# Kernel optimization log

Measured on AMD Instinct MI355X. Metric: run time of the kernel, lower is better.

The kernel has to match this reference:

```python
import jax, jax.numpy as jnp
import numpy as np

DILATION = 64
KERNEL = 2

def setup_inputs() -> dict:
    key = jax.random.key(0)
    k1, k2 = jax.random.split(key)
    x = jax.random.normal(k1, (16, 64, 16384), dtype=jnp.float32)
    w = jax.random.normal(k2, (64, 64, KERNEL), dtype=jnp.float32) * 0.1
    return {"x": x, "w": w}

def _causal_dilated_conv(x, w):
    # left-pad by dilation*(kernel_size-1) for causality
    pad = DILATION * (KERNEL - 1)
    xp = jnp.pad(x, ((0, 0), (0, 0), (pad, 0)))
    return jax.lax.conv_general_dilated(
        xp, w,
        window_strides=(1,),
        padding='VALID',
        rhs_dilation=(DILATION,),
        dimension_numbers=('NCH', 'OIH', 'NCH'))

def reference(x, w):
    y = _causal_dilated_conv(x, w)          # [B, C_out, T]
    return jnp.tanh(y) * jax.nn.sigmoid(y)  # fused gate
```

## Files before the change

### kernel.cpp

```cpp
#include <hip/hip_runtime.h>


#define B_ 16
#define C_ 64
#define T_ 16384
#define TT 128
#define HALO 64
#define RR (TT + HALO)

typedef __attribute__((ext_vector_type(8))) short short8;
typedef __attribute__((ext_vector_type(4))) float f32x4;

union Frag { short8 s; unsigned u[4]; };

__device__ __forceinline__ unsigned bf16_rne(float f) {
    unsigned u = __float_as_uint(f);
    return (u + 0x7fffu + ((u >> 16) & 1u)) >> 16;
}

__device__ __forceinline__ unsigned pack_rne(float a, float b) {
    unsigned ua = __float_as_uint(a), ub = __float_as_uint(b);
    unsigned ra = ua + 0x7fffu + ((ua >> 16) & 1u);
    unsigned rb = ub + 0x7fffu + ((ub >> 16) & 1u);
    return (ra >> 16) | (rb & 0xffff0000u);
}

__global__ __launch_bounds__(256, 6) void conv_gate_mfma3(
    const float* __restrict__ x,
    const float* __restrict__ w,
    float* __restrict__ out)
{
    __shared__ unsigned short xs[RR * 64];

    const int tid = threadIdx.x;
    const int t0  = blockIdx.x * TT;
    const int b   = blockIdx.y;
    const float* xb = x + (size_t)b * C_ * T_;

    #pragma unroll
    for (int it = 0; it < 6; ++it) {
        int task = it * 256 + tid;
        int rr   = task % RR;
        int c8   = task / RR;
        int g    = t0 - HALO + rr;
        float v[8];
        if (g >= 0) {
            const float* xp = xb + (size_t)(8 * c8) * T_ + g;
            #pragma unroll
            for (int i = 0; i < 8; ++i) v[i] = xp[(size_t)i * T_];
        } else {
            #pragma unroll
            for (int i = 0; i < 8; ++i) v[i] = 0.f;
        }
        unsigned p0 = pack_rne(v[0], v[1]);
        unsigned p1 = pack_rne(v[2], v[3]);
        unsigned p2 = pack_rne(v[4], v[5]);
        unsigned p3 = pack_rne(v[6], v[7]);
        int so = rr * 64 + ((c8 ^ (rr & 7)) * 8);
        *(uint4*)(&xs[so]) = make_uint4(p0, p1, p2, p3);
    }

    const int lane = tid & 63;
    const int wid  = tid >> 6;
    const int m    = lane & 15;
    const int q    = lane >> 4;
    const int co   = wid * 16 + m;

    Frag wh[2][2], wl[2][2];
    #pragma unroll
    for (int h = 0; h < 2; ++h) {
        const float* wp = w + co * 128 + h * 64 + q * 16;
        float f[16];
        #pragma unroll
        for (int v4 = 0; v4 < 4; ++v4) {
            float4 t4 = *(const float4*)(wp + 4 * v4);
            f[4*v4+0] = t4.x; f[4*v4+1] = t4.y; f[4*v4+2] = t4.z; f[4*v4+3] = t4.w;
        }
        #pragma unroll
        for (int p = 0; p < 2; ++p) {
            #pragma unroll
            for (int d = 0; d < 4; ++d) {
                float e0 = f[2*(2*d)   + p];
                float e1 = f[2*(2*d+1) + p];
                unsigned h0 = bf16_rne(e0), h1 = bf16_rne(e1);
                float r0 = e0 - __uint_as_float(h0 << 16);
                float r1 = e1 - __uint_as_float(h1 << 16);
                wh[p][h].u[d] = h0 | (h1 << 16);
                wl[p][h].u[d] = bf16_rne(r0) | (bf16_rne(r1) << 16);
            }
        }
    }

    f32x4 acc[8];
    #pragma unroll
    for (int s = 0; s < 8; ++s) acc[s] = (f32x4){0.f, 0.f, 0.f, 0.f};

    __syncthreads();

    const int n  = m;
    const int sw = n & 7;
    #pragma unroll
    for (int u = 0; u < 12; ++u) {
        const int rbase = (16 * u + n) * 64;
        Frag f0, f1;
        f0.s = *(const short8*)(&xs[rbase + ((q ^ sw) * 8)]);
        f1.s = *(const short8*)(&xs[rbase + (((4 + q) ^ sw) * 8)]);
        if (u < 8) {
            acc[u] = __builtin_amdgcn_mfma_f32_16x16x32_bf16(wh[0][0].s, f0.s, acc[u], 0, 0, 0);
            acc[u] = __builtin_amdgcn_mfma_f32_16x16x32_bf16(wl[0][0].s, f0.s, acc[u], 0, 0, 0);
            acc[u] = __builtin_amdgcn_mfma_f32_16x16x32_bf16(wh[0][1].s, f1.s, acc[u], 0, 0, 0);
            acc[u] = __builtin_amdgcn_mfma_f32_16x16x32_bf16(wl[0][1].s, f1.s, acc[u], 0, 0, 0);
        }
        if (u >= 4) {
            const int s2 = u - 4;
            acc[s2] = __builtin_amdgcn_mfma_f32_16x16x32_bf16(wh[1][0].s, f0.s, acc[s2], 0, 0, 0);
            acc[s2] = __builtin_amdgcn_mfma_f32_16x16x32_bf16(wl[1][0].s, f0.s, acc[s2], 0, 0, 0);
            acc[s2] = __builtin_amdgcn_mfma_f32_16x16x32_bf16(wh[1][1].s, f1.s, acc[s2], 0, 0, 0);
            acc[s2] = __builtin_amdgcn_mfma_f32_16x16x32_bf16(wl[1][1].s, f1.s, acc[s2], 0, 0, 0);
        }
    }

    float* ob = out + ((size_t)b * C_ + wid * 16) * T_ + t0;
    #pragma unroll
    for (int s = 0; s < 8; ++s) {
        #pragma unroll
        for (int r = 0; r < 4; ++r) {
            float y  = acc[s][r];
            y = fminf(fmaxf(y, -20.f), 20.f);
            float e   = __expf(-y);
            float e2  = e * e;
            float num = 1.f - e2;
            float den = (1.f + e) * (1.f + e2);
            ob[(size_t)(4 * q + r) * T_ + 16 * s + n] = num * __builtin_amdgcn_rcpf(den);
        }
    }
}

extern "C" void kernel_launch(void* const* d_in, const int* in_sizes, int n_in,
                              void* d_out, int out_size, void* d_ws, size_t ws_size,
                              hipStream_t stream) {
    const float* x = (const float*)d_in[0];
    const float* w = (const float*)d_in[1];
    float* out = (float*)d_out;
    dim3 grid(T_ / TT, B_);
    conv_gate_mfma3<<<grid, dim3(256), 0, stream>>>(x, w, out);
}
```

Before: 123.8 us.

## Stream time tiles through an LDS ring buffer with software-pipelined loads

Each block now handles 256 time steps in four 64-step chunks. It keeps a 128-row LDS ring, so the 64-sample halo is reused instead of reloaded. Global loads for the next chunk are issued before the MFMAs of the current chunk, and the previous chunk's gate epilogue is interleaved with them. Block IDs are remapped to spread work across XCDs. This cuts the halo re-read overhead and overlaps memory with compute, at the cost of extra barriers, higher register pressure (occupancy hint lowered to 4) and fewer blocks (1024).

```diff
diff --git a/kernel.cpp b/kernel.cpp
--- a/kernel.cpp
+++ b/kernel.cpp
@@ -4,9 +4,7 @@
 #define B_ 16
 #define C_ 64
 #define T_ 16384
-#define TT 128
-#define HALO 64
-#define RR (TT + HALO)
+#define RING 128
 
 typedef __attribute__((ext_vector_type(8))) short short8;
 typedef __attribute__((ext_vector_type(4))) float f32x4;
@@ -25,39 +23,52 @@
     return (ra >> 16) | (rb & 0xffff0000u);
 }
 
-__global__ __launch_bounds__(256, 6) void conv_gate_mfma3(
+#define EPILOGUE(A, KK)                                                     \
+    _Pragma("unroll")                                                       \
+    for (int s = 0; s < 4; ++s) {                                           \
+        _Pragma("unroll")                                                   \
+        for (int r = 0; r < 4; ++r) {                                       \
+            float y = (A)[s][r];                                            \
+            y = fminf(fmaxf(y, -20.f), 20.f);                               \
+            float e   = __expf(-y);                                         \
+            float e2  = e * e;                                              \
+            float num = 1.f - e2;                                           \
+            float den = (1.f + e) * (1.f + e2);                             \
+            ob[(size_t)(4 * q + r) * T_ + ((KK) * 64 + 16 * s + n)] =       \
+                num * __builtin_amdgcn_rcpf(den);                           \
+        }                                                                   \
+    }
+
+__global__ __launch_bounds__(256, 4) void conv_gate_ring(
     const float* __restrict__ x,
     const float* __restrict__ w,
     float* __restrict__ out)
 {
-    __shared__ unsigned short xs[RR * 64];
+    __shared__ unsigned short xs[RING * 64];
 
     const int tid = threadIdx.x;
-    const int t0  = blockIdx.x * TT;
-    const int b   = blockIdx.y;
+    const int bid = blockIdx.x;
+    const int wg  = (bid & 7) * 128 + (bid >> 3);
+    const int b   = wg >> 6;
+    const int seg = wg & 63;
+    const int t0  = seg << 8;
     const float* xb = x + (size_t)b * C_ * T_;
 
+    float pv[4][8];
     #pragma unroll
-    for (int it = 0; it < 6; ++it) {
-        int task = it * 256 + tid;
-        int rr   = task % RR;
-        int c8   = task / RR;
-        int g    = t0 - HALO + rr;
-        float v[8];
+    for (int it = 0; it < 4; ++it) {
+        const int task = it * 256 + tid;
+        const int rr   = task & 127;
+        const int c8   = task >> 7;
+        const int g    = t0 - 64 + rr;
         if (g >= 0) {
             const float* xp = xb + (size_t)(8 * c8) * T_ + g;
             #pragma unroll
-            for (int i = 0; i < 8; ++i) v[i] = xp[(size_t)i * T_];
+            for (int i = 0; i < 8; ++i) pv[it][i] = xp[(size_t)i * T_];
         } else {
             #pragma unroll
-            for (int i = 0; i < 8; ++i) v[i] = 0.f;
+            for (int i = 0; i < 8; ++i) pv[it][i] = 0.f;
         }
-        unsigned p0 = pack_rne(v[0], v[1]);
-        unsigned p1 = pack_rne(v[2], v[3]);
-        unsigned p2 = pack_rne(v[4], v[5]);
-        unsigned p3 = pack_rne(v[6], v[7]);
-        int so = rr * 64 + ((c8 ^ (rr & 7)) * 8);
-        *(uint4*)(&xs[so]) = make_uint4(p0, p1, p2, p3);
     }
 
     const int lane = tid & 63;
@@ -91,49 +102,89 @@
         }
     }
 
-    f32x4 acc[8];
     #pragma unroll
-    for (int s = 0; s < 8; ++s) acc[s] = (f32x4){0.f, 0.f, 0.f, 0.f};
+    for (int it = 0; it < 4; ++it) {
+        const int task = it * 256 + tid;
+        const int rr   = task & 127;
+        const int c8   = task >> 7;
+        unsigned p0 = pack_rne(pv[it][0], pv[it][1]);
+        unsigned p1 = pack_rne(pv[it][2], pv[it][3]);
+        unsigned p2 = pack_rne(pv[it][4], pv[it][5]);
+        unsigned p3 = pack_rne(pv[it][6], pv[it][7]);
+        const int slot = (rr + 64) & 127;
+        const int so   = slot * 64 + ((c8 ^ (rr & 7)) * 8);
+        *(uint4*)(&xs[so]) = make_uint4(p0, p1, p2, p3);
+    }
+
+    const int n   = m;
+    const int swb = n & 7;
+    float* ob = out + ((size_t)b * C_ + wid * 16) * T_ + t0;
+
+    f32x4 acc2[2][4];
 
     __syncthreads();
 
-    const int n  = m;
-    const int sw = n & 7;
     #pragma unroll
-    for (int u = 0; u < 12; ++u) {
-        const int rbase = (16 * u + n) * 64;
-        Frag f0, f1;
-        f0.s = *(const short8*)(&xs[rbase + ((q ^ sw) * 8)]);
-        f1.s = *(const short8*)(&xs[rbase + (((4 + q) ^ sw) * 8)]);
-        if (u < 8) {
-            acc[u] = __builtin_amdgcn_mfma_f32_16x16x32_bf16(wh[0][0].s, f0.s, acc[u], 0, 0, 0);
-            acc[u] = __builtin_amdgcn_mfma_f32_16x16x32_bf16(wl[0][0].s, f0.s, acc[u], 0, 0, 0);
-            acc[u] = __builtin_amdgcn_mfma_f32_16x16x32_bf16(wh[0][1].s, f1.s, acc[u], 0, 0, 0);
-            acc[u] = __builtin_amdgcn_mfma_f32_16x16x32_bf16(wl[0][1].s, f1.s, acc[u], 0, 0, 0);
+    for (int k = 0; k < 4; ++k) {
+        float v[2][8];
+        if (k < 3) {
+            #pragma unroll
+            for (int it = 0; it < 2; ++it) {
+                const int task = it * 256 + tid;
+                const int rr = task & 63, c8 = task >> 6;
+                const float* xp = xb + (size_t)(8 * c8) * T_ + (t0 + 64 * (k + 1) + rr);
+                #pragma unroll
+                for (int i = 0; i < 8; ++i) v[it][i] = xp[(size_t)i * T_];
+            }
         }
-        if (u >= 4) {
-            const int s2 = u - 4;
-            acc[s2] = __builtin_amdgcn_mfma_f32_16x16x32_bf16(wh[1][0].s, f0.s, acc[s2], 0, 0, 0);
-            acc[s2] = __builtin_amdgcn_mfma_f32_16x16x32_bf16(wl[1][0].s, f0.s, acc[s2], 0, 0, 0);
-            acc[s2] = __builtin_amdgcn_mfma_f32_16x16x32_bf16(wh[1][1].s, f1.s, acc[s2], 0, 0, 0);
-            acc[s2] = __builtin_amdgcn_mfma_f32_16x16x32_bf16(wl[1][1].s, f1.s, acc[s2], 0, 0, 0);
+
+        if (k > 0) { EPILOGUE(acc2[(k & 1) ^ 1], k - 1); }
+
+        f32x4* acc = acc2[k & 1];
+        #pragma unroll
+        for (int s = 0; s < 4; ++s) acc[s] = (f32x4){0.f, 0.f, 0.f, 0.f};
+        const int kb = ((k & 1) ^ 1) << 6;
+        #pragma unroll
+        for (int u = 0; u < 8; ++u) {
+            const int rbase = ((kb + 16 * u + n) & 127) * 64;
+            Frag f0, f1;
+            f0.s = *(const short8*)(&xs[rbase + ((q ^ swb) * 8)]);
+            f1.s = *(const short8*)(&xs[rbase + (((4 + q) ^ swb) * 8)]);
+            if (u < 4) {
+                acc[u] = __builtin_amdgcn_mfma_f32_16x16x32_bf16(wh[0][0].s, f0.s, acc[u], 0, 0, 0);
+                acc[u] = __builtin_amdgcn_mfma_f32_16x16x32_bf16(wl[0][0].s, f0.s, acc[u], 0, 0, 0);
+                acc[u] = __builtin_amdgcn_mfma_f32_16x16x32_bf16(wh[0][1].s, f1.s, acc[u], 0, 0, 0);
+                acc[u] = __builtin_amdgcn_mfma_f32_16x16x32_bf16(wl[0][1].s, f1.s, acc[u], 0, 0, 0);
+            } else {
+                const int s2 = u - 4;
+                acc[s2] = __builtin_amdgcn_mfma_f32_16x16x32_bf16(wh[1][0].s, f0.s, acc[s2], 0, 0, 0);
+                acc[s2] = __builtin_amdgcn_mfma_f32_16x16x32_bf16(wl[1][0].s, f0.s, acc[s2], 0, 0, 0);
+                acc[s2] = __builtin_amdgcn_mfma_f32_16x16x32_bf16(wh[1][1].s, f1.s, acc[s2], 0, 0, 0);
+                acc[s2] = __builtin_amdgcn_mfma_f32_16x16x32_bf16(wl[1][1].s, f1.s, acc[s2], 0, 0, 0);
+            }
+        }
+
+        if (k < 3) {
+            __syncthreads();
+
+            #pragma unroll
+            for (int it = 0; it < 2; ++it) {
+                const int task = it * 256 + tid;
+                const int rr = task & 63, c8 = task >> 6;
+                unsigned p0 = pack_rne(v[it][0], v[it][1]);
+                unsigned p1 = pack_rne(v[it][2], v[it][3]);
+                unsigned p2 = pack_rne(v[it][4], v[it][5]);
+                unsigned p3 = pack_rne(v[it][6], v[it][7]);
+                const int slot = (64 * (k + 1) + rr) & 127;
+                const int so   = slot * 64 + ((c8 ^ (rr & 7)) * 8);
+                *(uint4*)(&xs[so]) = make_uint4(p0, p1, p2, p3);
+            }
+
+            __syncthreads();
         }
     }
 
-    float* ob = out + ((size_t)b * C_ + wid * 16) * T_ + t0;
-    #pragma unroll
-    for (int s = 0; s < 8; ++s) {
-        #pragma unroll
-        for (int r = 0; r < 4; ++r) {
-            float y  = acc[s][r];
-            y = fminf(fmaxf(y, -20.f), 20.f);
-            float e   = __expf(-y);
-            float e2  = e * e;
-            float num = 1.f - e2;
-            float den = (1.f + e) * (1.f + e2);
-            ob[(size_t)(4 * q + r) * T_ + 16 * s + n] = num * __builtin_amdgcn_rcpf(den);
-        }
-    }
+    EPILOGUE(acc2[1], 3);
 }
 
 extern "C" void kernel_launch(void* const* d_in, const int* in_sizes, int n_in,
@@ -142,6 +193,5 @@
     const float* x = (const float*)d_in[0];
     const float* w = (const float*)d_in[1];
     float* out = (float*)d_out;
-    dim3 grid(T_ / TT, B_);
-    conv_gate_mfma3<<<grid, dim3(256), 0, stream>>>(x, w, out);
+    conv_gate_ring<<<dim3(1024), dim3(256), 0, stream>>>(x, w, out);
 }
```

After: 126.3 us. About the same (+2.0%).

## Stream x directly into registers with rolling halo, dropping shared-memory staging

Applied to the files above, without the earlier changes.

The conv kernel no longer stages a bf16 tile in LDS. Each wave loads its MFMA B-fragments straight from global memory and keeps the dilated halo in a four-slot rolling register buffer, with a two-deep register prefetch of upcoming columns. Tiles grow to 256 timesteps (1024 blocks on a 1-D grid remapped in XCD-interleaved order), which removes the halo re-read and the __syncthreads barrier. In exchange, register pressure rises (launch bounds drop to 4), and each wave issues strided scalar global loads, so every wave now performs its own global reads.

```diff
diff --git a/kernel.cpp b/kernel.cpp
--- a/kernel.cpp
+++ b/kernel.cpp
@@ -4,9 +4,6 @@
 #define B_ 16
 #define C_ 64
 #define T_ 16384
-#define TT 128
-#define HALO 64
-#define RR (TT + HALO)
 
 typedef __attribute__((ext_vector_type(8))) short short8;
 typedef __attribute__((ext_vector_type(4))) float f32x4;
@@ -25,46 +22,27 @@
     return (ra >> 16) | (rb & 0xffff0000u);
 }
 
-__global__ __launch_bounds__(256, 6) void conv_gate_mfma3(
+__global__ __launch_bounds__(256, 4) void conv_gate_stream(
     const float* __restrict__ x,
     const float* __restrict__ w,
     float* __restrict__ out)
 {
-    __shared__ unsigned short xs[RR * 64];
-
     const int tid = threadIdx.x;
-    const int t0  = blockIdx.x * TT;
-    const int b   = blockIdx.y;
-    const float* xb = x + (size_t)b * C_ * T_;
-
-    #pragma unroll
-    for (int it = 0; it < 6; ++it) {
-        int task = it * 256 + tid;
-        int rr   = task % RR;
-        int c8   = task / RR;
-        int g    = t0 - HALO + rr;
-        float v[8];
-        if (g >= 0) {
-            const float* xp = xb + (size_t)(8 * c8) * T_ + g;
-            #pragma unroll
-            for (int i = 0; i < 8; ++i) v[i] = xp[(size_t)i * T_];
-        } else {
-            #pragma unroll
-            for (int i = 0; i < 8; ++i) v[i] = 0.f;
-        }
-        unsigned p0 = pack_rne(v[0], v[1]);
-        unsigned p1 = pack_rne(v[2], v[3]);
-        unsigned p2 = pack_rne(v[4], v[5]);
-        unsigned p3 = pack_rne(v[6], v[7]);
-        int so = rr * 64 + ((c8 ^ (rr & 7)) * 8);
-        *(uint4*)(&xs[so]) = make_uint4(p0, p1, p2, p3);
-    }
+    const int bid = blockIdx.x;
+    const int wg  = (bid & 7) * 128 + (bid >> 3);
+    const int b   = wg >> 6;
+    const int s   = wg & 63;
+    const int t0  = s << 8;
 
     const int lane = tid & 63;
     const int wid  = tid >> 6;
     const int m    = lane & 15;
     const int q    = lane >> 4;
     const int co   = wid * 16 + m;
+
+    const float* xb  = x + (size_t)b * C_ * T_;
+    const float* xh0 = xb + (size_t)(8 * q) * T_ + m;
+    const float* xh1 = xb + (size_t)(32 + 8 * q) * T_ + m;
 
     Frag wh[2][2], wl[2][2];
     #pragma unroll
@@ -91,47 +69,83 @@
         }
     }
 
-    f32x4 acc[8];
+    Frag pk[4][2];
+    if (s > 0) {
+        #pragma unroll
+        for (int jj = 0; jj < 4; ++jj) {
+            float v0[8], v1[8];
+            const float* p0 = xh0 + (t0 - 64 + 16 * jj);
+            const float* p1 = xh1 + (t0 - 64 + 16 * jj);
+            #pragma unroll
+            for (int i = 0; i < 8; ++i) {
+                v0[i] = p0[(size_t)i * T_];
+                v1[i] = p1[(size_t)i * T_];
+            }
+            #pragma unroll
+            for (int d = 0; d < 4; ++d) {
+                pk[jj][0].u[d] = pack_rne(v0[2*d], v0[2*d+1]);
+                pk[jj][1].u[d] = pack_rne(v1[2*d], v1[2*d+1]);
+            }
+        }
+    } else {
+        #pragma unroll
+        for (int jj = 0; jj < 4; ++jj) {
+            #pragma unroll
+            for (int d = 0; d < 4; ++d) { pk[jj][0].u[d] = 0u; pk[jj][1].u[d] = 0u; }
+        }
+    }
+
+    float fl[2][16];
     #pragma unroll
-    for (int s = 0; s < 8; ++s) acc[s] = (f32x4){0.f, 0.f, 0.f, 0.f};
-
-    __syncthreads();
-
-    const int n  = m;
-    const int sw = n & 7;
-    #pragma unroll
-    for (int u = 0; u < 12; ++u) {
-        const int rbase = (16 * u + n) * 64;
-        Frag f0, f1;
-        f0.s = *(const short8*)(&xs[rbase + ((q ^ sw) * 8)]);
-        f1.s = *(const short8*)(&xs[rbase + (((4 + q) ^ sw) * 8)]);
-        if (u < 8) {
-            acc[u] = __builtin_amdgcn_mfma_f32_16x16x32_bf16(wh[0][0].s, f0.s, acc[u], 0, 0, 0);
-            acc[u] = __builtin_amdgcn_mfma_f32_16x16x32_bf16(wl[0][0].s, f0.s, acc[u], 0, 0, 0);
-            acc[u] = __builtin_amdgcn_mfma_f32_16x16x32_bf16(wh[0][1].s, f1.s, acc[u], 0, 0, 0);
-            acc[u] = __builtin_amdgcn_mfma_f32_16x16x32_bf16(wl[0][1].s, f1.s, acc[u], 0, 0, 0);
-        }
-        if (u >= 4) {
-            const int s2 = u - 4;
-            acc[s2] = __builtin_amdgcn_mfma_f32_16x16x32_bf16(wh[1][0].s, f0.s, acc[s2], 0, 0, 0);
-            acc[s2] = __builtin_amdgcn_mfma_f32_16x16x32_bf16(wl[1][0].s, f0.s, acc[s2], 0, 0, 0);
-            acc[s2] = __builtin_amdgcn_mfma_f32_16x16x32_bf16(wh[1][1].s, f1.s, acc[s2], 0, 0, 0);
-            acc[s2] = __builtin_amdgcn_mfma_f32_16x16x32_bf16(wl[1][1].s, f1.s, acc[s2], 0, 0, 0);
+    for (int jj = 0; jj < 2; ++jj) {
+        const float* p0 = xh0 + (t0 + 16 * jj);
+        const float* p1 = xh1 + (t0 + 16 * jj);
+        #pragma unroll
+        for (int i = 0; i < 8; ++i) {
+            fl[jj][i]     = p0[(size_t)i * T_];
+            fl[jj][8 + i] = p1[(size_t)i * T_];
         }
     }
 
     float* ob = out + ((size_t)b * C_ + wid * 16) * T_ + t0;
+
     #pragma unroll
-    for (int s = 0; s < 8; ++s) {
+    for (int j = 0; j < 16; ++j) {
+        Frag n0, n1;
+        #pragma unroll
+        for (int d = 0; d < 4; ++d) {
+            n0.u[d] = pack_rne(fl[j & 1][2*d],     fl[j & 1][2*d + 1]);
+            n1.u[d] = pack_rne(fl[j & 1][8 + 2*d], fl[j & 1][8 + 2*d + 1]);
+        }
+        if (j < 14) {
+            const float* p0 = xh0 + (t0 + 16 * (j + 2));
+            const float* p1 = xh1 + (t0 + 16 * (j + 2));
+            #pragma unroll
+            for (int i = 0; i < 8; ++i) {
+                fl[j & 1][i]     = p0[(size_t)i * T_];
+                fl[j & 1][8 + i] = p1[(size_t)i * T_];
+            }
+        }
+        f32x4 acc = (f32x4){0.f, 0.f, 0.f, 0.f};
+        acc = __builtin_amdgcn_mfma_f32_16x16x32_bf16(wh[0][0].s, pk[j & 3][0].s, acc, 0, 0, 0);
+        acc = __builtin_amdgcn_mfma_f32_16x16x32_bf16(wl[0][0].s, pk[j & 3][0].s, acc, 0, 0, 0);
+        acc = __builtin_amdgcn_mfma_f32_16x16x32_bf16(wh[0][1].s, pk[j & 3][1].s, acc, 0, 0, 0);
+        acc = __builtin_amdgcn_mfma_f32_16x16x32_bf16(wl[0][1].s, pk[j & 3][1].s, acc, 0, 0, 0);
+        acc = __builtin_amdgcn_mfma_f32_16x16x32_bf16(wh[1][0].s, n0.s, acc, 0, 0, 0);
+        acc = __builtin_amdgcn_mfma_f32_16x16x32_bf16(wl[1][0].s, n0.s, acc, 0, 0, 0);
+        acc = __builtin_amdgcn_mfma_f32_16x16x32_bf16(wh[1][1].s, n1.s, acc, 0, 0, 0);
+        acc = __builtin_amdgcn_mfma_f32_16x16x32_bf16(wl[1][1].s, n1.s, acc, 0, 0, 0);
+        pk[j & 3][0] = n0;
+        pk[j & 3][1] = n1;
         #pragma unroll
         for (int r = 0; r < 4; ++r) {
-            float y  = acc[s][r];
+            float y = acc[r];
             y = fminf(fmaxf(y, -20.f), 20.f);
             float e   = __expf(-y);
             float e2  = e * e;
             float num = 1.f - e2;
             float den = (1.f + e) * (1.f + e2);
-            ob[(size_t)(4 * q + r) * T_ + 16 * s + n] = num * __builtin_amdgcn_rcpf(den);
+            ob[(size_t)(4 * q + r) * T_ + 16 * j + m] = num * __builtin_amdgcn_rcpf(den);
         }
     }
 }
@@ -142,6 +156,5 @@
     const float* x = (const float*)d_in[0];
     const float* w = (const float*)d_in[1];
     float* out = (float*)d_out;
-    dim3 grid(T_ / TT, B_);
-    conv_gate_mfma3<<<grid, dim3(256), 0, stream>>>(x, w, out);
+    conv_gate_stream<<<dim3(1024), dim3(256), 0, stream>>>(x, w, out);
 }
```

Measured after the change: 306.2 us. 2.47x slower.
